# Performance work log

Hardware: AMD Instinct MI355X
Metric: run time of the kernel (lower is better)

Reference implementation:

```python
import jax, jax.numpy as jnp
import numpy as np

B, Q, K = 4, 256, 1024          # batch, query_len, key_len
DQ, DK, DV, H = 512, 512, 512, 256  # query/key/value dims, num_hiddens


def setup_inputs() -> dict:
    key = jax.random.key(0)
    ks = jax.random.split(key, 7)
    return {
        "queries": jax.random.normal(ks[0], (B, Q, DQ), jnp.float32),
        "keys": jax.random.normal(ks[1], (B, K, DK), jnp.float32),
        "values": jax.random.normal(ks[2], (B, K, DV), jnp.float32),
        "valid_lens": jax.random.randint(ks[3], (B,), 1, K + 1),
        "Wq": jax.random.normal(ks[4], (H, DQ), jnp.float32) / np.sqrt(DQ).astype(np.float32),
        "Wk": jax.random.normal(ks[5], (H, DK), jnp.float32) / np.sqrt(DK).astype(np.float32),
        "wv": jax.random.normal(ks[6], (H,), jnp.float32) / np.sqrt(H).astype(np.float32),
    }


def reference(queries, keys, values, valid_lens, Wq, Wk, wv):
    # Linear projections (bias=False), torch Linear weight layout (out, in)
    q = jnp.einsum("bqd,hd->bqh", queries, Wq)          # (B, Q, H)
    k = jnp.einsum("bkd,hd->bkh", keys, Wk)             # (B, K, H)
    # Broadcast add -> tanh -> scalar score per (q, k) pair
    feats = jnp.tanh(q[:, :, None, :] + k[:, None, :, :])  # (B, Q, K, H)
    scores = jnp.einsum("bqkh,h->bqk", feats, wv)           # (B, Q, K)
    # masked_softmax with 1D valid_lens: mask applies along key axis per batch
    kv_len = scores.shape[-1]
    mask = jnp.arange(kv_len)[None, None, :] < valid_lens[:, None, None]  # (B,1,K)
    scores = jnp.where(mask, scores, jnp.float32(-1e6))
    attn = jax.nn.softmax(scores, axis=-1)               # (B, Q, K)
    # dropout is identity in eval mode
    return jnp.einsum("bqk,bkv->bqv", attn, values)      # (B, Q, DV)
```

## Files before the change

### kernel.cpp

```cpp
#include <hip/hip_runtime.h>
#include <stdint.h>


#define NB 4
#define NQ 256
#define NK 1024
#define ND 512
#define NH 256
#define QROWS 4
#define PJR 16
#define PJH 64

#define C2L2E 2.8853900817779268f
#define L2E   1.4426950408889634f

typedef float v2f __attribute__((ext_vector_type(2)));

__device__ void ff_vldec(const int* p, int* v) {
  bool ok = true;
  for (int i = 0; i < 4; ++i) { int x = p[i]; if (x < 1 || x > NK) ok = false; }
  if (ok) { for (int i = 0; i < 4; ++i) v[i] = p[i]; return; }
  ok = true;
  for (int i = 0; i < 4; ++i) {
    if (p[2 * i + 1] != 0) ok = false;
    int x = p[2 * i]; if (x < 1 || x > NK) ok = false;
  }
  if (ok) { for (int i = 0; i < 4; ++i) v[i] = p[2 * i]; return; }
  ok = true;
  for (int i = 0; i < 4; ++i) {
    union { int i; float f; } u; u.i = p[i];
    if (!(u.f >= 1.0f && u.f <= 1024.0f && u.f == floorf(u.f))) ok = false;
  }
  if (ok) {
    for (int i = 0; i < 4; ++i) { union { int i; float f; } u; u.i = p[i]; v[i] = (int)u.f; }
    return;
  }
  ok = true;
  for (int i = 0; i < 4; ++i) {
    union { long long l; double d; } u;
    u.l = ((long long)p[2 * i + 1] << 32) | (unsigned int)p[2 * i];
    if (!(u.d >= 1.0 && u.d <= 1024.0 && u.d == floor(u.d))) ok = false;
  }
  if (ok) {
    for (int i = 0; i < 4; ++i) {
      union { long long l; double d; } u;
      u.l = ((long long)p[2 * i + 1] << 32) | (unsigned int)p[2 * i];
      v[i] = (int)u.d;
    }
    return;
  }
  const uint16_t* hh = (const uint16_t*)p;
  const short*    s  = (const short*)p;
  ok = true;
  for (int i = 0; i < 4; ++i) { int x = s[i]; if (x < 1 || x > NK) ok = false; }
  if (ok) { for (int i = 0; i < 4; ++i) v[i] = s[i]; return; }
  ok = true;
  for (int i = 0; i < 4; ++i) {
    union { uint16_t u; _Float16 h; } u; u.u = hh[i];
    float f = (float)u.h;
    if (!(f >= 1.0f && f <= 1024.0f && f == floorf(f))) ok = false;
  }
  if (ok) {
    for (int i = 0; i < 4; ++i) {
      union { uint16_t u; _Float16 h; } u; u.u = hh[i];
      v[i] = (int)(float)u.h;
    }
    return;
  }
  ok = true;
  for (int i = 0; i < 4; ++i) {
    union { uint32_t u; float f; } u; u.u = ((uint32_t)hh[i]) << 16;
    if (!(u.f >= 1.0f && u.f <= 1028.0f)) ok = false;
  }
  if (ok) {
    for (int i = 0; i < 4; ++i) {
      union { uint32_t u; float f; } u; u.u = ((uint32_t)hh[i]) << 16;
      int x = (int)(u.f + 0.5f); if (x > NK) x = NK; v[i] = x;
    }
    return;
  }
  for (int i = 0; i < 4; ++i) v[i] = NK;
}

__global__ __launch_bounds__(256) void ff_wt(
    const float* __restrict__ Wq, const float* __restrict__ Wk,
    float* __restrict__ WTq, float* __restrict__ WTk)
{
  const int idx = blockIdx.x * 256 + threadIdx.x;
  const int d4 = idx & 127, h = idx >> 7;
  const float* src = blockIdx.y ? Wk : Wq;
  float*       dst = blockIdx.y ? WTk : WTq;
  float4 w = *(const float4*)(src + (size_t)h * ND + d4 * 4);
  w.x *= C2L2E; w.y *= C2L2E; w.z *= C2L2E; w.w *= C2L2E;
  *(float4*)(dst + ((size_t)d4 * NH + h) * 4) = w;
}

__global__ __launch_bounds__(256) void ff_proj(
    const float* __restrict__ q_in, const float* __restrict__ k_in,
    const float* __restrict__ WTq, const float* __restrict__ WTk,
    float* __restrict__ qp, float* __restrict__ kp)
{
  __shared__ float xs[PJR * ND];
  const int t  = threadIdx.x;
  const int rg = blockIdx.x >> 2;
  const int h0 = (blockIdx.x & 3) * PJH;
  const int gr0 = rg * PJR;
  const bool isq = gr0 < NB * NQ;
  const float* xin = isq ? (q_in + (size_t)gr0 * ND)
                         : (k_in + (size_t)(gr0 - NB * NQ) * ND);
  const float4* wt4 = (const float4*)(isq ? WTq : WTk);

  #pragma unroll
  for (int i = 0; i < 8; ++i)
    ((float4*)xs)[t + 256 * i] = ((const float4*)xin)[t + 256 * i];
  __syncthreads();

  const int L  = t & 63;
  const int rw = t >> 6;
  float a0 = 0.f, a1 = 0.f, a2 = 0.f, a3 = 0.f;
  const float4* xr = (const float4*)xs + (size_t)(4 * rw) * 128;

  #pragma unroll 4
  for (int d4 = 0; d4 < ND / 4; ++d4) {
    float4 w  = wt4[(size_t)d4 * NH + h0 + L];
    float4 x0 = xr[d4];
    float4 x1 = xr[128 + d4];
    float4 x2 = xr[256 + d4];
    float4 x3 = xr[384 + d4];
    a0 += w.x*x0.x + w.y*x0.y + w.z*x0.z + w.w*x0.w;
    a1 += w.x*x1.x + w.y*x1.y + w.z*x1.z + w.w*x1.w;
    a2 += w.x*x2.x + w.y*x2.y + w.z*x2.z + w.w*x2.w;
    a3 += w.x*x3.x + w.y*x3.y + w.z*x3.z + w.w*x3.w;
  }

  const int h = h0 + L;
  if (isq) {
    float* o = qp + (size_t)(gr0 + 4 * rw) * NH + h;
    o[0] = a0; o[NH] = a1; o[2 * NH] = a2; o[3 * NH] = a3;
  } else {
    const int g = gr0 - NB * NQ + 4 * rw;
    const int bb = g >> 10, k = g & (NK - 1);
    *(float4*)(kp + ((size_t)bb * NH + h) * NK + k) = make_float4(a0, a1, a2, a3);
  }
}

__global__ __launch_bounds__(1024) void ff_attn2(
    const float* __restrict__ qp, const float* __restrict__ kp,
    const float* __restrict__ vals, const int* __restrict__ vlraw,
    const float* __restrict__ wvp, float* __restrict__ pvpart,
    float* __restrict__ Sg)
{
  __shared__ float qs[NH * QROWS];
  __shared__ float ws[NH];
  __shared__ float st[512 * QROWS];
  __shared__ float psum[32];
  __shared__ float part[4 * QROWS * ND];

  const int t  = threadIdx.x;
  const int kh = blockIdx.x;
  const int q0 = blockIdx.y * QROWS;
  const int b  = blockIdx.z;

  {
    const float* qsrc = qp + ((size_t)b * NQ + q0) * NH;
    const int row = t >> 8, h = t & 255;
    qs[h * QROWS + row] = qsrc[t];
    if (t < NH) ws[t] = -2.0f * wvp[t];
  }
  __syncthreads();

  int vls[4];
  ff_vldec(vlraw, vls);
  const int vl = vls[b];

  const int kk = t & 511, rh = t >> 9;
  v2f acc = {0.f, 0.f};
  {
    const float* kvp = kp + (size_t)b * NH * NK + kh * 512 + kk;
    const float* qsp = qs + 2 * rh;
    #pragma unroll 8
    for (int h = 0; h < NH; ++h) {
      float kv = kvp[(size_t)h * NK];
      v2f kv2; kv2.x = kv; kv2.y = kv;
      v2f q2 = *(const v2f*)(qsp + h * QROWS);
      float w = ws[h];
      v2f w2; w2.x = w; w2.y = w;
      v2f u = q2 + kv2;
      v2f e;
      e.x = __builtin_amdgcn_exp2f(u.x);
      e.y = __builtin_amdgcn_exp2f(u.y);
      v2f one; one.x = 1.0f; one.y = 1.0f;
      v2f d = one + e;
      v2f r;
      r.x = __builtin_amdgcn_rcpf(d.x);
      r.y = __builtin_amdgcn_rcpf(d.y);
      acc += w2 * r;
    }
  }
  {
    const bool okm = (kh * 512 + kk) < vl;
    v2f E;
    E.x = okm ? __builtin_amdgcn_exp2f(acc.x * L2E) : 0.f;
    E.y = okm ? __builtin_amdgcn_exp2f(acc.y * L2E) : 0.f;
    *(v2f*)&st[kk * 4 + 2 * rh] = E;
    float sx = E.x, sy = E.y;
    for (int o = 32; o; o >>= 1) { sx += __shfl_xor(sx, o); sy += __shfl_xor(sy, o); }
    if ((t & 63) == 0) { psum[(t >> 6) * 2] = sx; psum[(t >> 6) * 2 + 1] = sy; }
  }
  __syncthreads();

  if (t < 4) {
    const int j = t & 1, base = (t >> 1) * 8;
    float S = 0.f;
    #pragma unroll
    for (int w = 0; w < 8; ++w) S += psum[(base + w) * 2 + j];
    Sg[(((size_t)b * 64 + blockIdx.y) * 4 + t) * 2 + kh] = S;
  }

  {
    const int kq = t >> 8, c2 = (t & 255) * 2;
    const float* vb = vals + (size_t)b * NK * ND
                    + (size_t)(kh * 512 + kq * 128) * ND + c2;
    v2f o0 = {0.f,0.f}, o1 = {0.f,0.f}, o2 = {0.f,0.f}, o3 = {0.f,0.f};
    #pragma unroll 8
    for (int k = 0; k < 128; ++k) {
      v2f vv = *(const v2f*)(vb + (size_t)k * ND);
      float4 a = *(const float4*)&st[(kq * 128 + k) * 4];
      v2f ax; ax.x = a.x; ax.y = a.x;
      v2f ay; ay.x = a.y; ay.y = a.y;
      v2f az; az.x = a.z; az.y = a.z;
      v2f aw; aw.x = a.w; aw.y = a.w;
      o0 += ax * vv; o1 += ay * vv; o2 += az * vv; o3 += aw * vv;
    }
    *(v2f*)&part[(size_t)(kq * 4 + 0) * ND + c2] = o0;
    *(v2f*)&part[(size_t)(kq * 4 + 1) * ND + c2] = o1;
    *(v2f*)&part[(size_t)(kq * 4 + 2) * ND + c2] = o2;
    *(v2f*)&part[(size_t)(kq * 4 + 3) * ND + c2] = o3;
  }
  __syncthreads();
  {
    const int r = t >> 8, c2 = (t & 255) * 2;
    v2f s = {0.f, 0.f};
    #pragma unroll
    for (int kq = 0; kq < 4; ++kq)
      s += *(const v2f*)&part[(size_t)(kq * 4 + r) * ND + c2];
    *(v2f*)&pvpart[(((size_t)kh * NB + b) * NQ + q0 + r) * ND + c2] = s;
  }
}

__global__ __launch_bounds__(256) void ff_comb(
    const float* __restrict__ pvpart, const float* __restrict__ Sg,
    float* __restrict__ out)
{
  const int bid = blockIdx.x;
  const int t = threadIdx.x;
  const float S = Sg[bid * 2] + Sg[bid * 2 + 1];
  const float rs = 1.0f / S;
  const int b = bid >> 8, q = bid & 255;
  const float* p0 = pvpart + ((size_t)b * NQ + q) * ND;
  const float* p1 = pvpart + ((size_t)(NB + b) * NQ + q) * ND;
  float2 a = *(const float2*)(p0 + t * 2);
  float2 c = *(const float2*)(p1 + t * 2);
  *(float2*)(out + ((size_t)b * NQ + q) * ND + t * 2)
      = make_float2((a.x + c.x) * rs, (a.y + c.y) * rs);
}

__global__ __launch_bounds__(1024) void ff_attn(
    const float* __restrict__ qp, const float* __restrict__ kp,
    const float* __restrict__ vals, const int* __restrict__ vlraw,
    const float* __restrict__ wvp, float* __restrict__ out)
{
  __shared__ float qs[NH * QROWS];
  __shared__ float ws[NH];
  __shared__ float st[NK * QROWS];
  __shared__ float pm[16], psm[16];
  __shared__ float part[4 * QROWS * ND];

  const int t  = threadIdx.x;
  const int q0 = blockIdx.x * QROWS;
  const int b  = blockIdx.y;

  {
    const float* qsrc = qp + ((size_t)b * NQ + q0) * NH;
    const int row = t >> 8, h = t & 255;
    qs[h * QROWS + row] = qsrc[t];
    if (t < NH) ws[t] = -2.0f * wvp[t];
  }
  __syncthreads();

  int vls[4];
  ff_vldec(vlraw, vls);
  const int vl = vls[b];

  v2f a01 = {0.f, 0.f}, a23 = {0.f, 0.f};
  {
    const float* kvp = kp + (size_t)b * NH * NK + t;
    #pragma unroll 8
    for (int h = 0; h < NH; ++h) {
      float kv = kvp[(size_t)h * NK];
      v2f kv2; kv2.x = kv; kv2.y = kv;
      v2f q01 = *(const v2f*)(qs + h * QROWS);
      v2f q23 = *(const v2f*)(qs + h * QROWS + 2);
      float w = ws[h];
      v2f w2; w2.x = w; w2.y = w;
      v2f u01 = q01 + kv2, u23 = q23 + kv2;
      v2f e01, e23;
      e01.x = __builtin_amdgcn_exp2f(u01.x);
      e01.y = __builtin_amdgcn_exp2f(u01.y);
      e23.x = __builtin_amdgcn_exp2f(u23.x);
      e23.y = __builtin_amdgcn_exp2f(u23.y);
      v2f one; one.x = 1.0f; one.y = 1.0f;
      v2f d01 = one + e01, d23 = one + e23;
      v2f r01, r23;
      r01.x = __builtin_amdgcn_rcpf(d01.x);
      r01.y = __builtin_amdgcn_rcpf(d01.y);
      r23.x = __builtin_amdgcn_rcpf(d23.x);
      r23.y = __builtin_amdgcn_rcpf(d23.y);
      a01 += w2 * r01;
      a23 += w2 * r23;
    }
  }
  {
    const bool okm = (t < vl);
    *(float4*)&st[t * 4] = make_float4(okm ? a01.x : -1e6f, okm ? a01.y : -1e6f,
                                       okm ? a23.x : -1e6f, okm ? a23.y : -1e6f);
  }
  __syncthreads();

  {
    const int wid = t >> 6, lane = t & 63;
    const int row = wid >> 2, seg = wid & 3;
    const int kb = seg * 256 + lane;
    float v0 = st[(kb      ) * 4 + row];
    float v1 = st[(kb +  64) * 4 + row];
    float v2 = st[(kb + 128) * 4 + row];
    float v3 = st[(kb + 192) * 4 + row];
    float m = fmaxf(fmaxf(v0, v1), fmaxf(v2, v3));
    for (int o = 32; o; o >>= 1) m = fmaxf(m, __shfl_xor(m, o));
    if (lane == 0) pm[wid] = m;
    __syncthreads();
    m = fmaxf(fmaxf(pm[row*4+0], pm[row*4+1]), fmaxf(pm[row*4+2], pm[row*4+3]));
    float e0 = __builtin_amdgcn_exp2f((v0 - m) * L2E);
    float e1 = __builtin_amdgcn_exp2f((v1 - m) * L2E);
    float e2 = __builtin_amdgcn_exp2f((v2 - m) * L2E);
    float e3 = __builtin_amdgcn_exp2f((v3 - m) * L2E);
    float sm = e0 + e1 + e2 + e3;
    for (int o = 32; o; o >>= 1) sm += __shfl_xor(sm, o);
    if (lane == 0) psm[wid] = sm;
    __syncthreads();
    const float S = psm[row*4+0] + psm[row*4+1] + psm[row*4+2] + psm[row*4+3];
    const float rr = 1.0f / S;
    st[(kb      ) * 4 + row] = e0 * rr;
    st[(kb +  64) * 4 + row] = e1 * rr;
    st[(kb + 128) * 4 + row] = e2 * rr;
    st[(kb + 192) * 4 + row] = e3 * rr;
  }
  __syncthreads();

  {
    const int kq = t >> 8, c2 = (t & 255) * 2;
    const float* vb = vals + (size_t)b * NK * ND + c2;
    v2f o0 = {0.f,0.f}, o1 = {0.f,0.f}, o2 = {0.f,0.f}, o3 = {0.f,0.f};
    const int k0 = kq * 256;
    #pragma unroll 8
    for (int k = k0; k < k0 + 256; ++k) {
      v2f vv = *(const v2f*)(vb + (size_t)k * ND);
      float4 a = *(const float4*)&st[k * 4];
      v2f ax; ax.x = a.x; ax.y = a.x;
      v2f ay; ay.x = a.y; ay.y = a.y;
      v2f az; az.x = a.z; az.y = a.z;
      v2f aw; aw.x = a.w; aw.y = a.w;
      o0 += ax * vv; o1 += ay * vv; o2 += az * vv; o3 += aw * vv;
    }
    float* pp = &part[(size_t)kq * QROWS * ND + c2];
    *(v2f*)(pp         ) = o0;
    *(v2f*)(pp +     ND) = o1;
    *(v2f*)(pp + 2 * ND) = o2;
    *(v2f*)(pp + 3 * ND) = o3;
  }
  __syncthreads();
  {
    const int r = t >> 8, c2 = (t & 255) * 2;
    const float* pp = &part[(size_t)r * ND + c2];
    v2f s = {0.f, 0.f};
    #pragma unroll
    for (int kq = 0; kq < 4; ++kq) s += *(const v2f*)(pp + (size_t)kq * QROWS * ND);
    *(v2f*)(out + ((size_t)b * NQ + q0 + r) * ND + c2) = s;
  }
}

extern "C" void kernel_launch(void* const* d_in, const int* in_sizes, int n_in,
                              void* d_out, int out_size, void* d_ws, size_t ws_size,
                              hipStream_t stream) {
  const float* queries = (const float*)d_in[0];
  const float* keys    = (const float*)d_in[1];
  const float* values  = (const float*)d_in[2];
  const int*   vlens   = (const int*)d_in[3];
  const float* Wq      = (const float*)d_in[4];
  const float* Wk      = (const float*)d_in[5];
  const float* wv      = (const float*)d_in[6];
  float* out = (float*)d_out;

  float* qp  = (float*)d_ws;
  float* kp  = qp  + (size_t)NB * NQ * NH;
  float* wtq = kp  + (size_t)NB * NH * NK;
  float* wtk = wtq + (size_t)(ND / 4) * NH * 4;
  float* pvp = wtk + (size_t)(ND / 4) * NH * 4;
  float* Sg  = pvp + (size_t)2 * NB * NQ * ND;
  const size_t need = ((size_t)(Sg - (float*)d_ws) + 2 * NB * NQ) * sizeof(float);

  ff_wt  <<<dim3(128, 2), 256, 0, stream>>>(Wq, Wk, wtq, wtk);
  ff_proj<<<dim3((NB * (NQ + NK) / PJR) * (NH / PJH)), 256, 0, stream>>>(
      queries, keys, wtq, wtk, qp, kp);
  if (ws_size >= need) {
    ff_attn2<<<dim3(2, NQ / QROWS, NB), 1024, 0, stream>>>(
        qp, kp, values, vlens, wv, pvp, Sg);
    ff_comb<<<dim3(NB * NQ), 256, 0, stream>>>(pvp, Sg, out);
  } else {
    ff_attn<<<dim3(NQ / QROWS, NB), 1024, 0, stream>>>(
        qp, kp, values, vlens, wv, out);
  }
}
```

Measured before the change: 196.9 us.

## Factor exp out of tanh scoring and pair hidden units to share one reciprocal

The projection kernel now stores exp2 of the projected q and k values. The score loop can then compute exp(q+k) as a product, which removes the transcendental exp from the Q*K*H inner loop. In the main attention kernel, two hidden units are combined into one fraction (w0/(1+a) + w1/(1+b) over a common denominator), so one reciprocal covers two terms and the weights are precomputed as a float4 table. The risk is overflow or underflow when exp2 of large projections is multiplied together, which could produce inf/NaN or lose accuracy compared with the direct sigmoid form.

```diff
diff --git a/kernel.cpp b/kernel.cpp
--- a/kernel.cpp
+++ b/kernel.cpp
@@ -132,6 +132,10 @@
     a2 += w.x*x2.x + w.y*x2.y + w.z*x2.z + w.w*x2.w;
     a3 += w.x*x3.x + w.y*x3.y + w.z*x3.z + w.w*x3.w;
   }
+  a0 = __builtin_amdgcn_exp2f(a0);
+  a1 = __builtin_amdgcn_exp2f(a1);
+  a2 = __builtin_amdgcn_exp2f(a2);
+  a3 = __builtin_amdgcn_exp2f(a3);
 
   const int h = h0 + L;
   if (isq) {
@@ -150,11 +154,11 @@
     const float* __restrict__ wvp, float* __restrict__ pvpart,
     float* __restrict__ Sg)
 {
-  __shared__ float qs[NH * QROWS];
-  __shared__ float ws[NH];
-  __shared__ float st[512 * QROWS];
-  __shared__ float psum[32];
-  __shared__ float part[4 * QROWS * ND];
+  __shared__ float  qs[NH * QROWS];
+  __shared__ float4 wsp[NH / 2];
+  __shared__ float  st[512 * QROWS];
+  __shared__ float  psum[32];
+  __shared__ float  part[4 * QROWS * ND];
 
   const int t  = threadIdx.x;
   const int kh = blockIdx.x;
@@ -165,7 +169,10 @@
     const float* qsrc = qp + ((size_t)b * NQ + q0) * NH;
     const int row = t >> 8, h = t & 255;
     qs[h * QROWS + row] = qsrc[t];
-    if (t < NH) ws[t] = -2.0f * wvp[t];
+    if (t < NH / 2) {
+      float w0 = wvp[2 * t], w1 = wvp[2 * t + 1];
+      wsp[t] = make_float4(-2.0f * w0, -2.0f * w1, -2.0f * (w0 + w1), 0.0f);
+    }
   }
   __syncthreads();
 
@@ -178,23 +185,29 @@
   {
     const float* kvp = kp + (size_t)b * NH * NK + kh * 512 + kk;
     const float* qsp = qs + 2 * rh;
-    #pragma unroll 8
-    for (int h = 0; h < NH; ++h) {
-      float kv = kvp[(size_t)h * NK];
-      v2f kv2; kv2.x = kv; kv2.y = kv;
-      v2f q2 = *(const v2f*)(qsp + h * QROWS);
-      float w = ws[h];
-      v2f w2; w2.x = w; w2.y = w;
-      v2f u = q2 + kv2;
-      v2f e;
-      e.x = __builtin_amdgcn_exp2f(u.x);
-      e.y = __builtin_amdgcn_exp2f(u.y);
+    #pragma unroll 4
+    for (int hp = 0; hp < NH / 2; ++hp) {
+      float Ak0 = kvp[(size_t)(2 * hp) * NK];
+      float Ak1 = kvp[(size_t)(2 * hp + 1) * NK];
+      v2f Aq0 = *(const v2f*)(qsp + (2 * hp) * QROWS);
+      v2f Aq1 = *(const v2f*)(qsp + (2 * hp + 1) * QROWS);
+      float4 wt = wsp[hp];
+      v2f ak0; ak0.x = Ak0; ak0.y = Ak0;
+      v2f ak1; ak1.x = Ak1; ak1.y = Ak1;
+      v2f a = Aq0 * ak0;
+      v2f bb = Aq1 * ak1;
       v2f one; one.x = 1.0f; one.y = 1.0f;
-      v2f d = one + e;
-      v2f r;
-      r.x = __builtin_amdgcn_rcpf(d.x);
-      r.y = __builtin_amdgcn_rcpf(d.y);
-      acc += w2 * r;
+      v2f oa = one + a, ob = one + bb;
+      v2f D = oa * ob;
+      v2f w0s; w0s.x = wt.x; w0s.y = wt.x;
+      v2f w1s; w1s.x = wt.y; w1s.y = wt.y;
+      v2f N; N.x = wt.z; N.y = wt.z;
+      N += w0s * bb;
+      N += w1s * a;
+      v2f rD;
+      rD.x = __builtin_amdgcn_rcpf(D.x);
+      rD.y = __builtin_amdgcn_rcpf(D.y);
+      acc += N * rD;
     }
   }
   {
@@ -297,20 +310,15 @@
     const float* kvp = kp + (size_t)b * NH * NK + t;
     #pragma unroll 8
     for (int h = 0; h < NH; ++h) {
-      float kv = kvp[(size_t)h * NK];
-      v2f kv2; kv2.x = kv; kv2.y = kv;
+      float Ak = kvp[(size_t)h * NK];
+      v2f ak; ak.x = Ak; ak.y = Ak;
       v2f q01 = *(const v2f*)(qs + h * QROWS);
       v2f q23 = *(const v2f*)(qs + h * QROWS + 2);
       float w = ws[h];
       v2f w2; w2.x = w; w2.y = w;
-      v2f u01 = q01 + kv2, u23 = q23 + kv2;
-      v2f e01, e23;
-      e01.x = __builtin_amdgcn_exp2f(u01.x);
-      e01.y = __builtin_amdgcn_exp2f(u01.y);
-      e23.x = __builtin_amdgcn_exp2f(u23.x);
-      e23.y = __builtin_amdgcn_exp2f(u23.y);
       v2f one; one.x = 1.0f; one.y = 1.0f;
-      v2f d01 = one + e01, d23 = one + e23;
+      v2f d01 = one + q01 * ak;
+      v2f d23 = one + q23 * ak;
       v2f r01, r23;
       r01.x = __builtin_amdgcn_rcpf(d01.x);
       r01.y = __builtin_amdgcn_rcpf(d01.y);
```

Result: faster. 188.1 us (-4.5%).
